# Kernel optimization log

Hardware: AMD Instinct MI355X
Metric: run time of the kernel (lower is better)

Reference implementation:

```python
import jax, jax.numpy as jnp
import numpy as np

N_SLICES = 2  # init kwarg n_slices


def affine_grid_3d(theta, D, H, W):
    """torch.nn.functional.affine_grid for 5D output, align_corners=False.
    theta: [B,3,4]; returns grid [B,D,H,W,3] with last dim (x,y,z) ~ (W,H,D)."""
    xs = (jnp.arange(W, dtype=theta.dtype) + 0.5) * (2.0 / W) - 1.0
    ys = (jnp.arange(H, dtype=theta.dtype) + 0.5) * (2.0 / H) - 1.0
    zs = (jnp.arange(D, dtype=theta.dtype) + 0.5) * (2.0 / D) - 1.0
    zz, yy, xx = jnp.meshgrid(zs, ys, xs, indexing='ij')
    base = jnp.stack([xx, yy, zz, jnp.ones_like(xx)], axis=-1)  # [D,H,W,4]
    return jnp.einsum('bij,dhwj->bdhwi', theta, base)  # [B,D,H,W,3]


def grid_sample_3d_zeros(vol, grid):
    """torch.nn.functional.grid_sample, mode='bilinear' (trilinear for 5D),
    padding_mode='zeros', align_corners=False.
    vol: [B,C,D,H,W]; grid: [B,D,H,W,3] normalized xyz coords."""
    B, C, D, H, W = vol.shape
    ix = ((grid[..., 0] + 1.0) * W - 1.0) * 0.5
    iy = ((grid[..., 1] + 1.0) * H - 1.0) * 0.5
    iz = ((grid[..., 2] + 1.0) * D - 1.0) * 0.5
    ix0 = jnp.floor(ix); iy0 = jnp.floor(iy); iz0 = jnp.floor(iz)
    fx = ix - ix0; fy = iy - iy0; fz = iz - iz0

    def gather(v, z, y, x):  # v: [C,D,H,W], idx: [D,H,W] -> [C,D,H,W]
        return v[:, z, y, x]

    out = jnp.zeros((B, C, D, H, W), vol.dtype)
    for dz in (0, 1):
        for dy in (0, 1):
            for dx in (0, 1):
                xi = ix0 + dx; yi = iy0 + dy; zi = iz0 + dz
                w = (jnp.where(dx, fx, 1.0 - fx)
                     * jnp.where(dy, fy, 1.0 - fy)
                     * jnp.where(dz, fz, 1.0 - fz))
                valid = ((xi >= 0) & (xi < W) & (yi >= 0) & (yi < H)
                         & (zi >= 0) & (zi < D))
                xc = jnp.clip(xi, 0, W - 1).astype(jnp.int32)
                yc = jnp.clip(yi, 0, H - 1).astype(jnp.int32)
                zc = jnp.clip(zi, 0, D - 1).astype(jnp.int32)
                vals = jax.vmap(gather)(vol, zc, yc, xc)  # [B,C,D,H,W]
                out = out + vals * (w * valid)[:, None]
    return out


def skip_connector(x, b_grid_affines):
    B, C, SPAT, _ = x.shape
    # zero volume with the 2D slice stack placed at the central W-plane
    vol = jnp.zeros((B, C, SPAT, SPAT, SPAT), x.dtype).at[..., SPAT // 2].set(x)
    chunks = jnp.split(vol, N_SLICES, axis=1)
    outs = []
    for i in range(N_SLICES):
        aff = b_grid_affines[i].astype(jnp.float32)  # [B,4,4]
        # get_zooms: column norms of rotation block
        zooms = jnp.sqrt((aff[:, :3, :3] ** 2).sum(axis=1))  # [B,3]
        # rescale_rot_components_with_diag(aff, 1/zooms) == aff @ diag(1/zx,1/zy,1/zz,1)
        scale = jnp.concatenate([1.0 / zooms, jnp.ones((aff.shape[0], 1), aff.dtype)], axis=1)
        aff = aff * scale[:, None, :]
        theta = jnp.linalg.inv(aff)[:, :3, :]  # [B,3,4]
        grid = affine_grid_3d(theta, SPAT, SPAT, SPAT)
        outs.append(grid_sample_3d_zeros(chunks[i], grid))
    return jnp.concatenate(outs, axis=1)  # [B,C,SPAT,SPAT,SPAT]


def setup_inputs() -> dict:
    key = jax.random.key(0)
    k1, k2 = jax.random.split(key)
    B, C, SPAT = 2, 32, 96
    x = jax.random.normal(k1, (B, C, SPAT, SPAT), dtype=jnp.float32)
    # near-identity invertible homogeneous affines for the two views (SA, HLA)
    noise = 0.1 * jax.random.normal(k2, (2, B, 4, 4), dtype=jnp.float32)
    aff = jnp.eye(4, dtype=jnp.float32)[None, None] + noise
    aff = aff.at[..., 3, :].set(jnp.array([0.0, 0.0, 0.0, 1.0], dtype=jnp.float32))
    return {"x": x, "b_grid_affines": aff}


def reference(x, b_grid_affines):
    return skip_connector(x, b_grid_affines)
```

## Files before the change

### kernel.cpp

```cpp
#include <hip/hip_runtime.h>
#include <math.h>

#define SPAT  96
#define IMG   (SPAT*SPAT)
#define PLANE (SPAT*SPAT*SPAT)
#define TILE4 (IMG/4)

__device__ inline void invert4(const float m[16], float inv[16]) {
    inv[0]  =  m[5]*m[10]*m[15] - m[5]*m[11]*m[14] - m[9]*m[6]*m[15] + m[9]*m[7]*m[14] + m[13]*m[6]*m[11] - m[13]*m[7]*m[10];
    inv[4]  = -m[4]*m[10]*m[15] + m[4]*m[11]*m[14] + m[8]*m[6]*m[15] - m[8]*m[7]*m[14] - m[12]*m[6]*m[11] + m[12]*m[7]*m[10];
    inv[8]  =  m[4]*m[9]*m[15]  - m[4]*m[11]*m[13] - m[8]*m[5]*m[15] + m[8]*m[7]*m[13] + m[12]*m[5]*m[11] - m[12]*m[7]*m[9];
    inv[12] = -m[4]*m[9]*m[14]  + m[4]*m[10]*m[13] + m[8]*m[5]*m[14] - m[8]*m[6]*m[13] - m[12]*m[5]*m[10] + m[12]*m[6]*m[9];
    inv[1]  = -m[1]*m[10]*m[15] + m[1]*m[11]*m[14] + m[9]*m[2]*m[15] - m[9]*m[3]*m[14] - m[13]*m[2]*m[11] + m[13]*m[3]*m[10];
    inv[5]  =  m[0]*m[10]*m[15] - m[0]*m[11]*m[14] - m[8]*m[2]*m[15] + m[8]*m[3]*m[14] + m[12]*m[2]*m[11] - m[12]*m[3]*m[10];
    inv[9]  = -m[0]*m[9]*m[15]  + m[0]*m[11]*m[13] + m[8]*m[1]*m[15] - m[8]*m[3]*m[13] - m[12]*m[1]*m[11] + m[12]*m[3]*m[9];
    inv[13] =  m[0]*m[9]*m[14]  - m[0]*m[10]*m[13] - m[8]*m[1]*m[14] + m[8]*m[2]*m[13] + m[12]*m[1]*m[10] - m[12]*m[2]*m[9];
    inv[2]  =  m[1]*m[6]*m[15]  - m[1]*m[7]*m[14]  - m[5]*m[2]*m[15] + m[5]*m[3]*m[14] + m[13]*m[2]*m[7]  - m[13]*m[3]*m[6];
    inv[6]  = -m[0]*m[6]*m[15]  + m[0]*m[7]*m[14]  + m[4]*m[2]*m[15] - m[4]*m[3]*m[14] - m[12]*m[2]*m[7]  + m[12]*m[3]*m[6];
    inv[10] =  m[0]*m[5]*m[15]  - m[0]*m[7]*m[13]  - m[4]*m[1]*m[15] + m[4]*m[3]*m[13] + m[12]*m[1]*m[7]  - m[12]*m[3]*m[5];
    inv[14] = -m[0]*m[5]*m[14]  + m[0]*m[6]*m[13]  + m[4]*m[1]*m[14] - m[4]*m[2]*m[13] - m[12]*m[1]*m[6]  + m[12]*m[2]*m[5];
    inv[3]  = -m[1]*m[6]*m[11]  + m[1]*m[7]*m[10]  + m[5]*m[2]*m[11] - m[5]*m[3]*m[10] - m[9]*m[2]*m[7]   + m[9]*m[3]*m[6];
    inv[7]  =  m[0]*m[6]*m[11]  - m[0]*m[7]*m[10]  - m[4]*m[2]*m[11] + m[4]*m[3]*m[10] + m[8]*m[2]*m[7]   - m[8]*m[3]*m[6];
    inv[11] = -m[0]*m[5]*m[11]  + m[0]*m[7]*m[9]   + m[4]*m[1]*m[11] - m[4]*m[3]*m[9]  - m[8]*m[1]*m[7]   + m[8]*m[3]*m[5];
    inv[15] =  m[0]*m[5]*m[10]  - m[0]*m[6]*m[9]   - m[4]*m[1]*m[10] + m[4]*m[2]*m[9]  + m[8]*m[1]*m[6]   - m[8]*m[2]*m[5];
    float det  = m[0]*inv[0] + m[1]*inv[4] + m[2]*inv[8] + m[3]*inv[12];
    float rdet = 1.0f / det;
    for (int i = 0; i < 16; ++i) inv[i] *= rdet;
}

__global__ __launch_bounds__(256) void fused3_kernel(
        const float* __restrict__ xin,
        const float* __restrict__ aff_in,
        float4* __restrict__ out) {
    __shared__ float4 tile[TILE4];
    __shared__ float  Ms[12];
    const int tid = (int)threadIdx.x;
    const int d   = blockIdx.x;
    const int cc  = blockIdx.y;
    const int b   = cc >> 5;
    const int s   = (cc >> 4) & 1;
    const int sb  = s * 2 + b;

    if (tid == 0) {
        float A[16];
        #pragma unroll
        for (int i = 0; i < 16; ++i) A[i] = aff_in[sb * 16 + i];
        #pragma unroll
        for (int j = 0; j < 3; ++j) {
            float z = sqrtf(A[0*4+j]*A[0*4+j] + A[1*4+j]*A[1*4+j] + A[2*4+j]*A[2*4+j]);
            float rz = 1.0f / z;
            #pragma unroll
            for (int i = 0; i < 4; ++i) A[i*4+j] *= rz;
        }
        float inv[16];
        invert4(A, inv);
        #pragma unroll
        for (int r = 0; r < 3; ++r) {
            float T0 = inv[r*4+0], T1 = inv[r*4+1], T2 = inv[r*4+2], T3 = inv[r*4+3];
            Ms[r*4+0] = T0;
            Ms[r*4+1] = T1;
            Ms[r*4+2] = T2;
            Ms[r*4+3] = -47.5f * (T0 + T1 + T2) + 48.0f * T3 + 47.5f;
        }
    }
    const float4 z4 = make_float4(0.f, 0.f, 0.f, 0.f);
    #pragma unroll
    for (int it = 0; it < 9; ++it)
        tile[tid + 256 * it] = z4;

    __syncthreads();

    if (tid < SPAT) {
        const int h = tid;
        const float Mxw = Ms[0], Mxh = Ms[1], Mxd = Ms[2],  Mx0 = Ms[3];
        const float Myw = Ms[4], Myh = Ms[5], Myd = Ms[6],  My0 = Ms[7];
        const float Mzw = Ms[8], Mzh = Ms[9], Mzd = Ms[10], Mz0 = Ms[11];

        const float fh = (float)h, fd = (float)d;
        const float bx = Mxh * fh + Mxd * fd + Mx0;

        int wlo, whi;
        if (fabsf(Mxw) > 1e-6f) {
            float rMxw = 1.0f / Mxw;
            float w1 = (47.0f - bx) * rMxw;
            float w2 = (49.0f - bx) * rMxw;
            float wmin = fminf(w1, w2), wmax = fmaxf(w1, w2);
            wlo = max((int)ceilf(wmin), 0);
            whi = min((int)floorf(wmax), SPAT - 1);
        } else {
            bool in = fabsf(bx - 48.0f) < 1.0f;
            wlo = in ? 0 : 1;
            whi = in ? SPAT - 1 : 0;
        }
        if (wlo <= whi) {
            const float by = Myh * fh + Myd * fd + My0;
            const float bz = Mzh * fh + Mzd * fd + Mz0;
            const float* img = xin + (size_t)cc * IMG;

            const int qlo = wlo >> 2, qhi = whi >> 2;
            for (int q = qlo; q <= qhi; ++q) {
                float vv[4];
                #pragma unroll
                for (int j = 0; j < 4; ++j) {
                    float fw = (float)(4 * q + j);
                    float ix = Mxw * fw + bx;
                    float wx = 1.0f - fabsf(ix - 48.0f);
                    float r = 0.0f;
                    if (wx > 0.0f) {
                        float iy = Myw * fw + by;
                        float iz = Mzw * fw + bz;
                        float yf = floorf(iy), zf = floorf(iz);
                        float fy = iy - yf,    fz = iz - zf;
                        int y0 = (int)yf, z0 = (int)zf;
                        bool vy0 = (y0 >= 0)  & (y0 <  SPAT);
                        bool vy1 = (y0 >= -1) & (y0 <  SPAT - 1);
                        bool vz0 = (z0 >= 0)  & (z0 <  SPAT);
                        bool vz1 = (z0 >= -1) & (z0 <  SPAT - 1);
                        int y0c = min(max(y0, 0),     SPAT - 1);
                        int y1c = min(max(y0 + 1, 0), SPAT - 1);
                        int z0c = min(max(z0, 0),     SPAT - 1);
                        int z1c = min(max(z0 + 1, 0), SPAT - 1);
                        float wy0 = 1.0f - fy, wy1 = fy;
                        float wz0 = 1.0f - fz, wz1 = fz;
                        float w00 = wx * wz0 * wy0 * ((vz0 & vy0) ? 1.0f : 0.0f);
                        float w01 = wx * wz0 * wy1 * ((vz0 & vy1) ? 1.0f : 0.0f);
                        float w10 = wx * wz1 * wy0 * ((vz1 & vy0) ? 1.0f : 0.0f);
                        float w11 = wx * wz1 * wy1 * ((vz1 & vy1) ? 1.0f : 0.0f);
                        r = w00 * img[z0c * SPAT + y0c] + w01 * img[z0c * SPAT + y1c]
                          + w10 * img[z1c * SPAT + y0c] + w11 * img[z1c * SPAT + y1c];
                    }
                    vv[j] = r;
                }
                tile[h * 24 + q] = make_float4(vv[0], vv[1], vv[2], vv[3]);
            }
        }
    }

    __syncthreads();

    float4* op = out + ((size_t)cc * (PLANE / 4) + (size_t)d * (IMG / 4));
    #pragma unroll
    for (int it = 0; it < 9; ++it)
        op[tid + 256 * it] = tile[tid + 256 * it];
}

extern "C" void kernel_launch(void* const* d_in, const int* in_sizes, int n_in,
                              void* d_out, int out_size, void* d_ws, size_t ws_size,
                              hipStream_t stream) {
    const float* x   = (const float*)d_in[0];
    const float* aff = (const float*)d_in[1];
    float* out = (float*)d_out;

    dim3 grid(SPAT, 64);
    fused3_kernel<<<grid, 256, 0, stream>>>(x, aff, (float4*)out);
}
```

Baseline: 223.5 us.

## Split d-planes into half-row blocks and prefetch gathers before sync

Each block now handles half of a d-plane (48 h-rows), which doubles the grid and halves the shared tile. Every thread computes the affine matrix redundantly, so the single-thread setup plus sync is gone. Two threads per row each issue the gather loads for one quad before the tile-zeroing barrier, overlapping global latency with zeroing. Any remaining quads are computed in a serial loop as before. This adds register pressure and duplicated setup math, and sets launch bounds to 4 blocks per CU.

```diff
diff --git a/kernel.cpp b/kernel.cpp
--- a/kernel.cpp
+++ b/kernel.cpp
@@ -4,7 +4,8 @@
 #define SPAT  96
 #define IMG   (SPAT*SPAT)
 #define PLANE (SPAT*SPAT*SPAT)
-#define TILE4 (IMG/4)
+#define HROWS 48
+#define HCHUNK (HROWS*24)
 
 __device__ inline void invert4(const float m[16], float inv[16]) {
     inv[0]  =  m[5]*m[10]*m[15] - m[5]*m[11]*m[14] - m[9]*m[6]*m[15] + m[9]*m[7]*m[14] + m[13]*m[6]*m[11] - m[13]*m[7]*m[10];
@@ -28,20 +29,22 @@
     for (int i = 0; i < 16; ++i) inv[i] *= rdet;
 }
 
-__global__ __launch_bounds__(256) void fused3_kernel(
+__global__ __launch_bounds__(256, 4) void fused4_kernel(
         const float* __restrict__ xin,
         const float* __restrict__ aff_in,
         float4* __restrict__ out) {
-    __shared__ float4 tile[TILE4];
-    __shared__ float  Ms[12];
+    __shared__ float4 tile[HCHUNK];
     const int tid = (int)threadIdx.x;
-    const int d   = blockIdx.x;
+    const int dh2 = blockIdx.x;
+    const int d   = dh2 >> 1;
+    const int hh  = dh2 & 1;
     const int cc  = blockIdx.y;
     const int b   = cc >> 5;
     const int s   = (cc >> 4) & 1;
     const int sb  = s * 2 + b;
 
-    if (tid == 0) {
+    float M[12];
+    {
         float A[16];
         #pragma unroll
         for (int i = 0; i < 16; ++i) A[i] = aff_in[sb * 16 + i];
@@ -57,27 +60,30 @@
         #pragma unroll
         for (int r = 0; r < 3; ++r) {
             float T0 = inv[r*4+0], T1 = inv[r*4+1], T2 = inv[r*4+2], T3 = inv[r*4+3];
-            Ms[r*4+0] = T0;
-            Ms[r*4+1] = T1;
-            Ms[r*4+2] = T2;
-            Ms[r*4+3] = -47.5f * (T0 + T1 + T2) + 48.0f * T3 + 47.5f;
-        }
-    }
-    const float4 z4 = make_float4(0.f, 0.f, 0.f, 0.f);
-    #pragma unroll
-    for (int it = 0; it < 9; ++it)
-        tile[tid + 256 * it] = z4;
-
-    __syncthreads();
-
-    if (tid < SPAT) {
-        const int h = tid;
-        const float Mxw = Ms[0], Mxh = Ms[1], Mxd = Ms[2],  Mx0 = Ms[3];
-        const float Myw = Ms[4], Myh = Ms[5], Myd = Ms[6],  My0 = Ms[7];
-        const float Mzw = Ms[8], Mzh = Ms[9], Mzd = Ms[10], Mz0 = Ms[11];
-
+            M[r*4+0] = T0;
+            M[r*4+1] = T1;
+            M[r*4+2] = T2;
+            M[r*4+3] = -47.5f * (T0 + T1 + T2) + 48.0f * T3 + 47.5f;
+        }
+    }
+    const float Mxw = M[0], Mxh = M[1], Mxd = M[2],  Mx0 = M[3];
+    const float Myw = M[4], Myh = M[5], Myd = M[6],  My0 = M[7];
+    const float Mzw = M[8], Mzh = M[9], Mzd = M[10], Mz0 = M[11];
+
+    const float* img = xin + (size_t)cc * IMG;
+
+    float tv[16];
+    float bx = 0.f, by = 0.f, bz = 0.f;
+    int   rr = 0, myq = 0, fqlo = 0, fqhi = -1;
+    bool  act = false;
+    if (tid < 2 * HROWS) {
+        rr = tid >> 1;
+        const int k = tid & 1;
+        const int h = hh * HROWS + rr;
         const float fh = (float)h, fd = (float)d;
-        const float bx = Mxh * fh + Mxd * fd + Mx0;
+        bx = Mxh * fh + Mxd * fd + Mx0;
+        by = Myh * fh + Myd * fd + My0;
+        bz = Mzh * fh + Mzd * fd + Mz0;
 
         int wlo, whi;
         if (fabsf(Mxw) > 1e-6f) {
@@ -92,56 +98,115 @@
             wlo = in ? 0 : 1;
             whi = in ? SPAT - 1 : 0;
         }
-        if (wlo <= whi) {
-            const float by = Myh * fh + Myd * fd + My0;
-            const float bz = Mzh * fh + Mzd * fd + Mz0;
-            const float* img = xin + (size_t)cc * IMG;
-
-            const int qlo = wlo >> 2, qhi = whi >> 2;
-            for (int q = qlo; q <= qhi; ++q) {
-                float vv[4];
-                #pragma unroll
-                for (int j = 0; j < 4; ++j) {
-                    float fw = (float)(4 * q + j);
-                    float ix = Mxw * fw + bx;
-                    float wx = 1.0f - fabsf(ix - 48.0f);
-                    float r = 0.0f;
-                    if (wx > 0.0f) {
-                        float iy = Myw * fw + by;
-                        float iz = Mzw * fw + bz;
-                        float yf = floorf(iy), zf = floorf(iz);
-                        float fy = iy - yf,    fz = iz - zf;
-                        int y0 = (int)yf, z0 = (int)zf;
-                        bool vy0 = (y0 >= 0)  & (y0 <  SPAT);
-                        bool vy1 = (y0 >= -1) & (y0 <  SPAT - 1);
-                        bool vz0 = (z0 >= 0)  & (z0 <  SPAT);
-                        bool vz1 = (z0 >= -1) & (z0 <  SPAT - 1);
-                        int y0c = min(max(y0, 0),     SPAT - 1);
-                        int y1c = min(max(y0 + 1, 0), SPAT - 1);
-                        int z0c = min(max(z0, 0),     SPAT - 1);
-                        int z1c = min(max(z0 + 1, 0), SPAT - 1);
-                        float wy0 = 1.0f - fy, wy1 = fy;
-                        float wz0 = 1.0f - fz, wz1 = fz;
-                        float w00 = wx * wz0 * wy0 * ((vz0 & vy0) ? 1.0f : 0.0f);
-                        float w01 = wx * wz0 * wy1 * ((vz0 & vy1) ? 1.0f : 0.0f);
-                        float w10 = wx * wz1 * wy0 * ((vz1 & vy0) ? 1.0f : 0.0f);
-                        float w11 = wx * wz1 * wy1 * ((vz1 & vy1) ? 1.0f : 0.0f);
-                        r = w00 * img[z0c * SPAT + y0c] + w01 * img[z0c * SPAT + y1c]
-                          + w10 * img[z1c * SPAT + y0c] + w11 * img[z1c * SPAT + y1c];
-                    }
-                    vv[j] = r;
+        const int qlo = wlo >> 2, qhi = whi >> 2;
+        myq = qlo + k;
+        if (wlo <= whi && myq <= qhi) {
+            act = true;
+            #pragma unroll
+            for (int j = 0; j < 4; ++j) {
+                float fw = (float)(4 * myq + j);
+                float ix = Mxw * fw + bx;
+                float wx = 1.0f - fabsf(ix - 48.0f);
+                if (wx > 0.0f) {
+                    float iy = Myw * fw + by;
+                    float iz = Mzw * fw + bz;
+                    int y0 = (int)floorf(iy), z0 = (int)floorf(iz);
+                    int y0c = min(max(y0, 0),     SPAT - 1);
+                    int y1c = min(max(y0 + 1, 0), SPAT - 1);
+                    int z0c = min(max(z0, 0),     SPAT - 1);
+                    int z1c = min(max(z0 + 1, 0), SPAT - 1);
+                    tv[4*j+0] = img[z0c * SPAT + y0c];
+                    tv[4*j+1] = img[z0c * SPAT + y1c];
+                    tv[4*j+2] = img[z1c * SPAT + y0c];
+                    tv[4*j+3] = img[z1c * SPAT + y1c];
+                } else {
+                    tv[4*j+0] = 0.f; tv[4*j+1] = 0.f;
+                    tv[4*j+2] = 0.f; tv[4*j+3] = 0.f;
                 }
-                tile[h * 24 + q] = make_float4(vv[0], vv[1], vv[2], vv[3]);
             }
         }
-    }
+        if (k == 1 && wlo <= whi) { fqlo = qlo + 2; fqhi = qhi; }
+    }
+
+    const float4 z4 = make_float4(0.f, 0.f, 0.f, 0.f);
+    #pragma unroll
+    for (int i = tid; i < HCHUNK; i += 256) tile[i] = z4;
 
     __syncthreads();
 
-    float4* op = out + ((size_t)cc * (PLANE / 4) + (size_t)d * (IMG / 4));
+    if (act) {
+        float vv[4];
+        #pragma unroll
+        for (int j = 0; j < 4; ++j) {
+            float fw = (float)(4 * myq + j);
+            float ix = Mxw * fw + bx;
+            float wx = 1.0f - fabsf(ix - 48.0f);
+            float r = 0.0f;
+            if (wx > 0.0f) {
+                float iy = Myw * fw + by;
+                float iz = Mzw * fw + bz;
+                float yf = floorf(iy), zf = floorf(iz);
+                float fy = iy - yf,    fz = iz - zf;
+                int y0 = (int)yf, z0 = (int)zf;
+                bool vy0 = (y0 >= 0)  & (y0 <  SPAT);
+                bool vy1 = (y0 >= -1) & (y0 <  SPAT - 1);
+                bool vz0 = (z0 >= 0)  & (z0 <  SPAT);
+                bool vz1 = (z0 >= -1) & (z0 <  SPAT - 1);
+                float wy0 = 1.0f - fy, wy1 = fy;
+                float wz0 = 1.0f - fz, wz1 = fz;
+                float w00 = wx * wz0 * wy0 * ((vz0 & vy0) ? 1.0f : 0.0f);
+                float w01 = wx * wz0 * wy1 * ((vz0 & vy1) ? 1.0f : 0.0f);
+                float w10 = wx * wz1 * wy0 * ((vz1 & vy0) ? 1.0f : 0.0f);
+                float w11 = wx * wz1 * wy1 * ((vz1 & vy1) ? 1.0f : 0.0f);
+                r = w00 * tv[4*j+0] + w01 * tv[4*j+1]
+                  + w10 * tv[4*j+2] + w11 * tv[4*j+3];
+            }
+            vv[j] = r;
+        }
+        tile[rr * 24 + myq] = make_float4(vv[0], vv[1], vv[2], vv[3]);
+    }
+    for (int q = fqlo; q <= fqhi; ++q) {
+        float vv[4];
+        #pragma unroll
+        for (int j = 0; j < 4; ++j) {
+            float fw = (float)(4 * q + j);
+            float ix = Mxw * fw + bx;
+            float wx = 1.0f - fabsf(ix - 48.0f);
+            float r = 0.0f;
+            if (wx > 0.0f) {
+                float iy = Myw * fw + by;
+                float iz = Mzw * fw + bz;
+                float yf = floorf(iy), zf = floorf(iz);
+                float fy = iy - yf,    fz = iz - zf;
+                int y0 = (int)yf, z0 = (int)zf;
+                bool vy0 = (y0 >= 0)  & (y0 <  SPAT);
+                bool vy1 = (y0 >= -1) & (y0 <  SPAT - 1);
+                bool vz0 = (z0 >= 0)  & (z0 <  SPAT);
+                bool vz1 = (z0 >= -1) & (z0 <  SPAT - 1);
+                int y0c = min(max(y0, 0),     SPAT - 1);
+                int y1c = min(max(y0 + 1, 0), SPAT - 1);
+                int z0c = min(max(z0, 0),     SPAT - 1);
+                int z1c = min(max(z0 + 1, 0), SPAT - 1);
+                float wy0 = 1.0f - fy, wy1 = fy;
+                float wz0 = 1.0f - fz, wz1 = fz;
+                float w00 = wx * wz0 * wy0 * ((vz0 & vy0) ? 1.0f : 0.0f);
+                float w01 = wx * wz0 * wy1 * ((vz0 & vy1) ? 1.0f : 0.0f);
+                float w10 = wx * wz1 * wy0 * ((vz1 & vy0) ? 1.0f : 0.0f);
+                float w11 = wx * wz1 * wy1 * ((vz1 & vy1) ? 1.0f : 0.0f);
+                r = w00 * img[z0c * SPAT + y0c] + w01 * img[z0c * SPAT + y1c]
+                  + w10 * img[z1c * SPAT + y0c] + w11 * img[z1c * SPAT + y1c];
+            }
+            vv[j] = r;
+        }
+        tile[rr * 24 + q] = make_float4(vv[0], vv[1], vv[2], vv[3]);
+    }
+
+    __syncthreads();
+
+    float4* op = out + ((size_t)cc * (PLANE / 4) + (size_t)d * (IMG / 4)
+                        + (size_t)hh * HCHUNK);
     #pragma unroll
-    for (int it = 0; it < 9; ++it)
-        op[tid + 256 * it] = tile[tid + 256 * it];
+    for (int i = tid; i < HCHUNK; i += 256) op[i] = tile[i];
 }
 
 extern "C" void kernel_launch(void* const* d_in, const int* in_sizes, int n_in,
@@ -151,6 +216,6 @@
     const float* aff = (const float*)d_in[1];
     float* out = (float*)d_out;
 
-    dim3 grid(SPAT, 64);
-    fused3_kernel<<<grid, 256, 0, stream>>>(x, aff, (float4*)out);
+    dim3 grid(2 * SPAT, 64);
+    fused4_kernel<<<grid, 256, 0, stream>>>(x, aff, (float4*)out);
 }
```

New measurement: 220.3 us. About the same (-1.4%).

## Shrink shared tile to sparse per-row slots and split rows across two threads

Applied to the files above, without the earlier changes.

Replaces the full 36KB shared-memory plane tile with three float4 slots per row plus a packed per-row range word, so more blocks can be resident per CU (launch bounds raised to 8). Each thread now computes the affine fold itself instead of one thread plus a barrier, and two threads share each row's nonzero chunks. Rows whose nonzero span exceeds three chunks are written straight to global memory. The final store pass rebuilds zeros from the range info. This adds per-thread redundant matrix inversion and more index arithmetic in the store loop.

```diff
diff --git a/kernel.cpp b/kernel.cpp
--- a/kernel.cpp
+++ b/kernel.cpp
@@ -4,7 +4,9 @@
 #define SPAT  96
 #define IMG   (SPAT*SPAT)
 #define PLANE (SPAT*SPAT*SPAT)
-#define TILE4 (IMG/4)
+#define KSLOT 3
+
+typedef float f32x4 __attribute__((ext_vector_type(4)));
 
 __device__ inline void invert4(const float m[16], float inv[16]) {
     inv[0]  =  m[5]*m[10]*m[15] - m[5]*m[11]*m[14] - m[9]*m[6]*m[15] + m[9]*m[7]*m[14] + m[13]*m[6]*m[11] - m[13]*m[7]*m[10];
@@ -28,12 +30,73 @@
     for (int i = 0; i < 16; ++i) inv[i] *= rdet;
 }
 
-__global__ __launch_bounds__(256) void fused3_kernel(
+__device__ inline void fold_affine(const float* __restrict__ aff_in, int sb,
+                                   float M[12]) {
+    float A[16];
+    #pragma unroll
+    for (int i = 0; i < 16; ++i) A[i] = aff_in[sb * 16 + i];
+    #pragma unroll
+    for (int j = 0; j < 3; ++j) {
+        float z = sqrtf(A[0*4+j]*A[0*4+j] + A[1*4+j]*A[1*4+j] + A[2*4+j]*A[2*4+j]);
+        float rz = 1.0f / z;
+        #pragma unroll
+        for (int i = 0; i < 4; ++i) A[i*4+j] *= rz;
+    }
+    float inv[16];
+    invert4(A, inv);
+    #pragma unroll
+    for (int r = 0; r < 3; ++r) {
+        float T0 = inv[r*4+0], T1 = inv[r*4+1], T2 = inv[r*4+2], T3 = inv[r*4+3];
+        M[r*4+0] = T0;
+        M[r*4+1] = T1;
+        M[r*4+2] = T2;
+        M[r*4+3] = -47.5f * (T0 + T1 + T2) + 48.0f * T3 + 47.5f;
+    }
+}
+
+__device__ inline f32x4 compose_chunk(int q, float bx, float by, float bz,
+        float Mxw, float Myw, float Mzw, const float* __restrict__ img) {
+    f32x4 v;
+    #pragma unroll
+    for (int j = 0; j < 4; ++j) {
+        float fw = (float)(4 * q + j);
+        float ix = Mxw * fw + bx;
+        float wx = 1.0f - fabsf(ix - 48.0f);
+        float r = 0.0f;
+        if (wx > 0.0f) {
+            float iy = Myw * fw + by;
+            float iz = Mzw * fw + bz;
+            float yf = floorf(iy), zf = floorf(iz);
+            float fy = iy - yf,    fz = iz - zf;
+            int y0 = (int)yf, z0 = (int)zf;
+            bool vy0 = (y0 >= 0)  & (y0 <  SPAT);
+            bool vy1 = (y0 >= -1) & (y0 <  SPAT - 1);
+            bool vz0 = (z0 >= 0)  & (z0 <  SPAT);
+            bool vz1 = (z0 >= -1) & (z0 <  SPAT - 1);
+            int y0c = min(max(y0, 0),     SPAT - 1);
+            int y1c = min(max(y0 + 1, 0), SPAT - 1);
+            int z0c = min(max(z0, 0),     SPAT - 1);
+            int z1c = min(max(z0 + 1, 0), SPAT - 1);
+            float wy0 = 1.0f - fy, wy1 = fy;
+            float wz0 = 1.0f - fz, wz1 = fz;
+            float w00 = wx * wz0 * wy0 * ((vz0 & vy0) ? 1.0f : 0.0f);
+            float w01 = wx * wz0 * wy1 * ((vz0 & vy1) ? 1.0f : 0.0f);
+            float w10 = wx * wz1 * wy0 * ((vz1 & vy0) ? 1.0f : 0.0f);
+            float w11 = wx * wz1 * wy1 * ((vz1 & vy1) ? 1.0f : 0.0f);
+            r = w00 * img[z0c * SPAT + y0c] + w01 * img[z0c * SPAT + y1c]
+              + w10 * img[z1c * SPAT + y0c] + w11 * img[z1c * SPAT + y1c];
+        }
+        v[j] = r;
+    }
+    return v;
+}
+
+__global__ __launch_bounds__(256, 8) void fused6_kernel(
         const float* __restrict__ xin,
         const float* __restrict__ aff_in,
-        float4* __restrict__ out) {
-    __shared__ float4 tile[TILE4];
-    __shared__ float  Ms[12];
+        f32x4* __restrict__ out) {
+    __shared__ f32x4    sval[SPAT * KSLOT];
+    __shared__ unsigned rinf[SPAT];
     const int tid = (int)threadIdx.x;
     const int d   = blockIdx.x;
     const int cc  = blockIdx.y;
@@ -41,41 +104,14 @@
     const int s   = (cc >> 4) & 1;
     const int sb  = s * 2 + b;
 
-    if (tid == 0) {
-        float A[16];
-        #pragma unroll
-        for (int i = 0; i < 16; ++i) A[i] = aff_in[sb * 16 + i];
-        #pragma unroll
-        for (int j = 0; j < 3; ++j) {
-            float z = sqrtf(A[0*4+j]*A[0*4+j] + A[1*4+j]*A[1*4+j] + A[2*4+j]*A[2*4+j]);
-            float rz = 1.0f / z;
-            #pragma unroll
-            for (int i = 0; i < 4; ++i) A[i*4+j] *= rz;
-        }
-        float inv[16];
-        invert4(A, inv);
-        #pragma unroll
-        for (int r = 0; r < 3; ++r) {
-            float T0 = inv[r*4+0], T1 = inv[r*4+1], T2 = inv[r*4+2], T3 = inv[r*4+3];
-            Ms[r*4+0] = T0;
-            Ms[r*4+1] = T1;
-            Ms[r*4+2] = T2;
-            Ms[r*4+3] = -47.5f * (T0 + T1 + T2) + 48.0f * T3 + 47.5f;
-        }
-    }
-    const float4 z4 = make_float4(0.f, 0.f, 0.f, 0.f);
-    #pragma unroll
-    for (int it = 0; it < 9; ++it)
-        tile[tid + 256 * it] = z4;
+    if (tid < 2 * SPAT) {
+        float M[12];
+        fold_affine(aff_in, sb, M);
+        const float Mxw = M[0], Mxh = M[1], Mxd = M[2],  Mx0 = M[3];
+        const float Myw = M[4], Myh = M[5], Myd = M[6],  My0 = M[7];
+        const float Mzw = M[8], Mzh = M[9], Mzd = M[10], Mz0 = M[11];
 
-    __syncthreads();
-
-    if (tid < SPAT) {
-        const int h = tid;
-        const float Mxw = Ms[0], Mxh = Ms[1], Mxd = Ms[2],  Mx0 = Ms[3];
-        const float Myw = Ms[4], Myh = Ms[5], Myd = Ms[6],  My0 = Ms[7];
-        const float Mzw = Ms[8], Mzh = Ms[9], Mzd = Ms[10], Mz0 = Ms[11];
-
+        const int h = tid >> 1, k = tid & 1;
         const float fh = (float)h, fd = (float)d;
         const float bx = Mxh * fh + Mxd * fd + Mx0;
 
@@ -92,56 +128,63 @@
             wlo = in ? 0 : 1;
             whi = in ? SPAT - 1 : 0;
         }
-        if (wlo <= whi) {
+        const int  qlo   = wlo >> 2, qhi = whi >> 2;
+        const bool empty = (wlo > whi);
+        const bool ovf   = !empty && ((qhi - qlo + 1) > KSLOT);
+        if (k == 0)
+            rinf[h] = empty ? 0xFFu
+                : ((unsigned)qlo | ((unsigned)qhi << 8) | (ovf ? 0x10000u : 0u));
+
+        if (!empty) {
             const float by = Myh * fh + Myd * fd + My0;
             const float bz = Mzh * fh + Mzd * fd + Mz0;
             const float* img = xin + (size_t)cc * IMG;
-
-            const int qlo = wlo >> 2, qhi = whi >> 2;
-            for (int q = qlo; q <= qhi; ++q) {
-                float vv[4];
-                #pragma unroll
-                for (int j = 0; j < 4; ++j) {
-                    float fw = (float)(4 * q + j);
-                    float ix = Mxw * fw + bx;
-                    float wx = 1.0f - fabsf(ix - 48.0f);
-                    float r = 0.0f;
-                    if (wx > 0.0f) {
-                        float iy = Myw * fw + by;
-                        float iz = Mzw * fw + bz;
-                        float yf = floorf(iy), zf = floorf(iz);
-                        float fy = iy - yf,    fz = iz - zf;
-                        int y0 = (int)yf, z0 = (int)zf;
-                        bool vy0 = (y0 >= 0)  & (y0 <  SPAT);
-                        bool vy1 = (y0 >= -1) & (y0 <  SPAT - 1);
-                        bool vz0 = (z0 >= 0)  & (z0 <  SPAT);
-                        bool vz1 = (z0 >= -1) & (z0 <  SPAT - 1);
-                        int y0c = min(max(y0, 0),     SPAT - 1);
-                        int y1c = min(max(y0 + 1, 0), SPAT - 1);
-                        int z0c = min(max(z0, 0),     SPAT - 1);
-                        int z1c = min(max(z0 + 1, 0), SPAT - 1);
-                        float wy0 = 1.0f - fy, wy1 = fy;
-                        float wz0 = 1.0f - fz, wz1 = fz;
-                        float w00 = wx * wz0 * wy0 * ((vz0 & vy0) ? 1.0f : 0.0f);
-                        float w01 = wx * wz0 * wy1 * ((vz0 & vy1) ? 1.0f : 0.0f);
-                        float w10 = wx * wz1 * wy0 * ((vz1 & vy0) ? 1.0f : 0.0f);
-                        float w11 = wx * wz1 * wy1 * ((vz1 & vy1) ? 1.0f : 0.0f);
-                        r = w00 * img[z0c * SPAT + y0c] + w01 * img[z0c * SPAT + y1c]
-                          + w10 * img[z1c * SPAT + y0c] + w11 * img[z1c * SPAT + y1c];
-                    }
-                    vv[j] = r;
-                }
-                tile[h * 24 + q] = make_float4(vv[0], vv[1], vv[2], vv[3]);
+            if (!ovf) {
+                const int myq = qlo + k;
+                if (myq <= qhi)
+                    sval[h * KSLOT + k] =
+                        compose_chunk(myq, bx, by, bz, Mxw, Myw, Mzw, img);
+                if (k == 1 && qlo + 2 <= qhi)
+                    sval[h * KSLOT + 2] =
+                        compose_chunk(qlo + 2, bx, by, bz, Mxw, Myw, Mzw, img);
+            } else {
+                f32x4* op = out + (size_t)cc * (PLANE / 4)
+                                + (size_t)d * (IMG / 4) + h * 24;
+                for (int q = qlo + k; q <= qhi; q += 2)
+                    op[q] = compose_chunk(q, bx, by, bz, Mxw, Myw, Mzw, img);
             }
         }
     }
 
     __syncthreads();
 
-    float4* op = out + ((size_t)cc * (PLANE / 4) + (size_t)d * (IMG / 4));
+    int hh[9], qq[9];
     #pragma unroll
-    for (int it = 0; it < 9; ++it)
-        op[tid + 256 * it] = tile[tid + 256 * it];
+    for (int it = 0; it < 9; ++it) {
+        const int tl = tid + 256 * it;
+        hh[it] = tl / 24;
+        qq[it] = tl - hh[it] * 24;
+    }
+
+    f32x4* op = out + (size_t)cc * (PLANE / 4) + (size_t)d * (IMG / 4);
+    #pragma unroll
+    for (int it = 0; it < 9; ++it) {
+        const unsigned info = rinf[hh[it]];
+        const unsigned qlo  = info & 0xFFu;
+        const unsigned qhi  = (info >> 8) & 0xFFu;
+        const unsigned q    = (unsigned)qq[it];
+        const bool ins = (q >= qlo) & (q <= qhi);
+        const bool ovf = (info & 0x10000u) != 0u;
+        const int slot = min(max((int)q - (int)qlo, 0), KSLOT - 1);
+        f32x4 sv = sval[hh[it] * KSLOT + slot];
+        f32x4 v;
+        v.x = ins ? sv.x : 0.f;
+        v.y = ins ? sv.y : 0.f;
+        v.z = ins ? sv.z : 0.f;
+        v.w = ins ? sv.w : 0.f;
+        if (!(ins && ovf))
+            op[tid + 256 * it] = v;
+    }
 }
 
 extern "C" void kernel_launch(void* const* d_in, const int* in_sizes, int n_in,
@@ -152,5 +195,5 @@
     float* out = (float*)d_out;
 
     dim3 grid(SPAT, 64);
-    fused3_kernel<<<grid, 256, 0, stream>>>(x, aff, (float4*)out);
+    fused6_kernel<<<grid, 256, 0, stream>>>(x, aff, (f32x4*)out);
 }
```

After: 221.4 us. About the same (-0.9%).
